# Performance work log

Measured on AMD Instinct MI355X. Metric: run time of the kernel, lower is better.

The kernel has to match this reference:

```python
import jax, jax.numpy as jnp
import numpy as np

T, F, C, V, H, E, S = 256, 32, 8, 10000, 1024, 256, 512
PAD, BOS, EOS = 0, 1, 2


def setup_inputs() -> dict:
    key = jax.random.key(0)
    ks = jax.random.split(key, 16)
    sH = 1.0 / np.sqrt(H).astype(np.float32)
    inp = {
        'token_ctx': jax.random.normal(ks[0], (1, S, H), jnp.float32),
        'char_emb_w': jax.random.normal(ks[1], (V, E), jnp.float32) * 0.02,
        'enc_W_ih': jax.random.normal(ks[2], (3 * H, E), jnp.float32) * sH,
        'enc_W_hh': jax.random.normal(ks[3], (3 * H, H), jnp.float32) * sH,
        'enc_b_ih': jnp.zeros((3 * H,), jnp.float32),
        'enc_b_hh': jnp.zeros((3 * H,), jnp.float32),
        'dec_W_ih': jax.random.normal(ks[4], (3 * H, E), jnp.float32) * sH,
        'dec_W_hh': jax.random.normal(ks[5], (3 * H, H), jnp.float32) * sH,
        'dec_b_ih': jnp.zeros((3 * H,), jnp.float32),
        'dec_b_hh': jnp.zeros((3 * H,), jnp.float32),
        'out_W': jax.random.normal(ks[6], (V, H), jnp.float32) * sH,
        'out_b': jnp.zeros((V,), jnp.float32),
    }
    # (token_id, xtoken_idx, char_id) triples; every token 1..T has exactly C chars
    tok_ids = jnp.repeat(jnp.arange(1, T + 1, dtype=jnp.int32), C)
    xt_ids = jax.random.randint(ks[7], (T * C,), 0, S, jnp.int32)
    ch_ids = jax.random.randint(ks[8], (T * C,), 4, V, jnp.int32)  # avoid specials
    inp['in_sent_token_chars'] = jnp.stack([tok_ids, xt_ids, ch_ids], axis=-1)[None]
    gold = jax.random.randint(ks[9], (T * F,), 4, V, jnp.int32)  # no EOS -> full-length decode
    inp['out_chars'] = jnp.concatenate([jnp.array([BOS], jnp.int32), gold])[None]
    inp['max_tokens'] = T
    inp['max_form_len'] = F
    inp['use_teacher_forcing'] = 1
    return inp


def _gru_cell(x, h, W_ih, W_hh, b_ih, b_hh):
    # PyTorch GRU cell convention; x:[T,E], h:[T,H]
    gi = x @ W_ih.T + b_ih
    gh = h @ W_hh.T + b_hh
    i_r, i_z, i_n = jnp.split(gi, 3, axis=-1)
    h_r, h_z, h_n = jnp.split(gh, 3, axis=-1)
    r = jax.nn.sigmoid(i_r + h_r)
    z = jax.nn.sigmoid(i_z + h_z)
    n = jnp.tanh(i_n + r * h_n)
    return (1.0 - z) * n + z * h


def reference(token_ctx, char_emb_w, enc_W_ih, enc_W_hh, enc_b_ih, enc_b_hh,
              dec_W_ih, dec_W_hh, dec_b_ih, dec_b_hh, out_W, out_b,
              in_sent_token_chars, out_chars, max_tokens, max_form_len,
              use_teacher_forcing):
    Vout = out_b.shape[0]
    # ragged mask select per token id -> here every token has exactly C chars
    tc = in_sent_token_chars[0].reshape(max_tokens, -1, 3)  # [T, C, 3]
    chars = tc[:, :, 2]          # [T, C]
    xtoken_ids = tc[:, :, 1]     # [T, C]
    # enc_state = mean over the token's xtoken contexts
    h0 = jnp.mean(token_ctx[0][xtoken_ids], axis=1)  # [T, H]
    # ---- encoder GRU over the token's chars (batched over tokens) ----
    x_enc = char_emb_w[chars]  # [T, C, E]

    def enc_step(h, x):
        return _gru_cell(x, h, enc_W_ih, enc_W_hh, enc_b_ih, enc_b_hh), None

    h_enc, _ = jax.lax.scan(enc_step, h0, jnp.swapaxes(x_enc, 0, 1))  # [T, H]
    # ---- decoder GRU, max_form_len steps, teacher-forced, EOS freeze+pad ----
    # gold char for token t at step s is out_chars[0, t*F + s + 1]
    gold = out_chars[0, 1:1 + max_tokens * max_form_len].reshape(max_tokens, max_form_len)
    c0 = jnp.full((max_tokens,), out_chars[0, 0], dtype=out_chars.dtype)
    done0 = (c0 == EOS)
    last0 = jnp.zeros((max_tokens, Vout), jnp.float32)

    def dec_step(carry, g):
        h, c, done, last = carry
        x = char_emb_w[c]
        h_new = _gru_cell(x, h, dec_W_ih, dec_W_hh, dec_b_ih, dec_b_hh)
        s_new = h_new @ out_W.T + out_b
        score = jnp.where(done[:, None], last, s_new)  # pad with last score after EOS
        h = jnp.where(done[:, None], h, h_new)         # state frozen after EOS
        if use_teacher_forcing:
            c_next = g
        else:
            c_next = jnp.argmax(s_new, axis=-1).astype(c.dtype)
        done = done | (c_next == EOS)
        return (h, c_next, done, score), score

    _, scores = jax.lax.scan(dec_step, (h_enc, c0, done0, last0),
                             jnp.swapaxes(gold, 0, 1))  # [F, T, V]
    # torch.cat(dec_scores, dim=1): token-major, step-minor -> [1, T*F, V]
    return jnp.transpose(scores, (1, 0, 2)).reshape(1, max_tokens * max_form_len, Vout)
```

## Files before the change

kernel.cpp:

```cpp
#include <hip/hip_runtime.h>
#include <hip/hip_bf16.h>
#include <math.h>

#define TT   256
#define FF   32
#define CCH  8
#define VV   10000
#define HH   1024
#define EE   256
#define NG   3072
#define EOS_ID 2
#define NSTEPS 40
#define CHAIN_BLKS 256
#define CTR_INTS 512

#define LDS_GP_OFF    98304
#define LDS_STB_OFF   (98304 + 53248)
#define LDS_TOTAL     (98304 + 53248 + 2048)

#define SC_LDS_TOTAL  131072

typedef __attribute__((ext_vector_type(8))) short bf16x8;
typedef __attribute__((ext_vector_type(4))) float f32x4;

__device__ __forceinline__ void gload_lds16(const void* g, void* l) {
    __builtin_amdgcn_global_load_lds((const __attribute__((address_space(1))) void*)g,
                                     (__attribute__((address_space(3))) void*)l,
                                     16, 0, 0);
}

__device__ __forceinline__ float sigmf(float x) { return 1.f / (1.f + __expf(-x)); }

__global__ __launch_bounds__(256) void prep_kernel(const int* __restrict__ oc,
                                                   int* __restrict__ c_in,
                                                   unsigned char* __restrict__ done,
                                                   int* __restrict__ ctr) {
    int t = threadIdx.x;
    for (int i = t; i < CTR_INTS; i += 256) ctr[i] = 0;
    int c0 = oc[0];
    bool d = (c0 == EOS_ID);
    for (int f = 0; f < FF; ++f) {
        c_in[t * FF + f] = (f == 0) ? c0 : oc[1 + t * FF + f - 1];
        done[t * FF + f] = d ? 1 : 0;
        d = d || (oc[1 + t * FF + f] == EOS_ID);
    }
}

__global__ __launch_bounds__(256) void h0_kernel(const float* __restrict__ tctx,
                                                 const int* __restrict__ sent,
                                                 float* __restrict__ h,
                                                 __hip_bfloat16* __restrict__ A0) {
    int t = blockIdx.x;
    int tid = threadIdx.x;
    __shared__ int xt[CCH];
    if (tid < CCH) xt[tid] = sent[(t * CCH + tid) * 3 + 1];
    __syncthreads();
#pragma unroll
    for (int jj = 0; jj < 4; ++jj) {
        int j = tid + jj * 256;
        float s = 0.f;
#pragma unroll
        for (int c = 0; c < CCH; ++c) s += tctx[(size_t)xt[c] * HH + j];
        float hv = s * 0.125f;
        h[(size_t)t * HH + j] = hv;
        A0[(size_t)t * HH + j] = __float2bfloat16(hv);
    }
}

__global__ __launch_bounds__(256) void f2b_kernel(const float* __restrict__ src,
                                                  __hip_bfloat16* __restrict__ dst) {
    size_t base = ((size_t)blockIdx.x * 256 + threadIdx.x) * 4;
    float4 v = *(const float4*)(src + base);
    dst[base + 0] = __float2bfloat16(v.x);
    dst[base + 1] = __float2bfloat16(v.y);
    dst[base + 2] = __float2bfloat16(v.z);
    dst[base + 3] = __float2bfloat16(v.w);
}

__global__ __launch_bounds__(256) void build_Bg2(const float* __restrict__ Whh,
                                                 __hip_bfloat16* __restrict__ Bg) {
    int by = blockIdx.x;
    int tid = threadIdx.x;
    int jb = by / 48, rr = by % 48;
    int g = rr >> 4, jj = rr & 15;
    const float* srow = Whh + (size_t)(g * 1024 + jb * 16 + jj) * HH;
    __hip_bfloat16* drow = Bg + (size_t)by * HH;
    float4 v = *(const float4*)(srow + tid * 4);
    drow[tid * 4 + 0] = __float2bfloat16(v.x);
    drow[tid * 4 + 1] = __float2bfloat16(v.y);
    drow[tid * 4 + 2] = __float2bfloat16(v.z);
    drow[tid * 4 + 3] = __float2bfloat16(v.w);
}

template<int MODE>
__global__ __launch_bounds__(256) void gemm_pipe(const __hip_bfloat16* __restrict__ A, int lda,
                                                 const __hip_bfloat16* __restrict__ B, int ldb,
                                                 __hip_bfloat16* __restrict__ Cb,
                                                 const int* __restrict__ idsrc,
                                                 int NIT) {
    __shared__ __hip_bfloat16 As[4][128 * 32];
    __shared__ __hip_bfloat16 Bs[4][128 * 32];
    __shared__ int sids[128];

    const int tid = threadIdx.x;
    const int n0 = blockIdx.x * 128;
    const int m0 = blockIdx.y * 128;

    if (tid < 128) {
        int row = m0 + tid;
        int t = row & 255;
        int id;
        if (MODE == 1) { int c = row >> 8; id = idsrc[(t * CCH + c) * 3 + 2]; }
        else           { int f = row >> 8; id = idsrc[t * FF + f]; }
        sids[tid] = id;
    }
    __syncthreads();

    const int srow = tid >> 2, skq = tid & 3;
    const int l = tid & 63;
    const int w = tid >> 6;
    const int wr = (w >> 1) * 64, wc = (w & 1) * 64;
    const int fra = ((wr + (l & 15)) << 5) + ((l >> 4) << 3);
    const int frb = ((wc + (l & 15)) << 5) + ((l >> 4) << 3);

    f32x4 acc[4][4];
#pragma unroll
    for (int i = 0; i < 4; ++i)
#pragma unroll
        for (int j = 0; j < 4; ++j) acc[i][j] = (f32x4){0.f, 0.f, 0.f, 0.f};

    auto stage = [&](int slot, int it) {
        const int k0 = it * 32;
        const __hip_bfloat16* ga0 = A + (size_t)sids[srow] * lda + k0 + skq * 8;
        const __hip_bfloat16* ga1 = A + (size_t)sids[64 + srow] * lda + k0 + skq * 8;
        const __hip_bfloat16* gb0 = B + (size_t)(n0 + srow) * ldb + k0 + skq * 8;
        const __hip_bfloat16* gb1 = B + (size_t)(n0 + 64 + srow) * ldb + k0 + skq * 8;
        __hip_bfloat16* lA = &As[slot][tid * 8];
        __hip_bfloat16* lB = &Bs[slot][tid * 8];
        gload_lds16(ga0, lA);
        gload_lds16(ga1, lA + 2048);
        gload_lds16(gb0, lB);
        gload_lds16(gb1, lB + 2048);
    };

    stage(0, 0);
    stage(1, 1);

    for (int it = 0; it < NIT; ++it) {
        if (it + 2 < NIT) stage((it + 2) & 3, it + 2);
        int ahead = NIT - 1 - it; if (ahead > 2) ahead = 2;
        if (ahead >= 2)      asm volatile("s_waitcnt vmcnt(8)" ::: "memory");
        else if (ahead == 1) asm volatile("s_waitcnt vmcnt(4)" ::: "memory");
        else                 asm volatile("s_waitcnt vmcnt(0)" ::: "memory");
        __builtin_amdgcn_s_barrier();
        __builtin_amdgcn_sched_barrier(0);

        const __hip_bfloat16* cA = As[it & 3];
        const __hip_bfloat16* cB = Bs[it & 3];
        bf16x8 af[4], bfv[4];
#pragma unroll
        for (int fm = 0; fm < 4; ++fm) af[fm] = *(const bf16x8*)&cA[fra + fm * 512];
#pragma unroll
        for (int fn = 0; fn < 4; ++fn) bfv[fn] = *(const bf16x8*)&cB[frb + fn * 512];
#pragma unroll
        for (int fm = 0; fm < 4; ++fm)
#pragma unroll
            for (int fn = 0; fn < 4; ++fn)
                acc[fm][fn] = __builtin_amdgcn_mfma_f32_16x16x32_bf16(af[fm], bfv[fn], acc[fm][fn], 0, 0, 0);
    }

    const int colb = wc + (l & 15);
    const int rb   = wr + ((l >> 4) << 2);
#pragma unroll
    for (int fm = 0; fm < 4; ++fm)
#pragma unroll
        for (int fn = 0; fn < 4; ++fn)
#pragma unroll
            for (int q = 0; q < 4; ++q)
                Cb[(size_t)(m0 + rb + fm * 16 + q) * NG + n0 + colb + fn * 16] =
                    __float2bfloat16(acc[fm][fn][q]);
}

__global__ __launch_bounds__(256, 1) void chain_kernel(
    __hip_bfloat16* Abuf0, __hip_bfloat16* Abuf1,
    const __hip_bfloat16* __restrict__ Bg_e,
    const __hip_bfloat16* __restrict__ Bg_d,
    const __hip_bfloat16* __restrict__ gi_enc, const __hip_bfloat16* __restrict__ gi_dec,
    const float* __restrict__ ebih, const float* __restrict__ ebhh,
    const float* __restrict__ dbih, const float* __restrict__ dbhh,
    const float* __restrict__ hA,
    __hip_bfloat16* __restrict__ hsb,
    const unsigned char* __restrict__ dflags,
    int* flags) {

    extern __shared__ __align__(16) char smem[];
    char* Bs = smem;
    float* gp = (float*)(smem + LDS_GP_OFF);
    __hip_bfloat16* stb = (__hip_bfloat16*)(smem + LDS_STB_OFF);

    const int tid = threadIdx.x;
    const int b = blockIdx.x;
    const int mt = b >> 6, jb = b & 63;
    const int m0 = mt * 64;
    const int jbase = jb * 16;

    const int l = tid & 63, w = tid >> 6;
    const int ji = tid & 15;
    const int rg = tid >> 4;
    const int j = jbase + ji;
    const int lrow = l & 15;
    const int lk8  = (l >> 4) << 3;

    float hreg[4];
#pragma unroll
    for (int p = 0; p < 4; ++p)
        hreg[p] = hA[(size_t)(m0 + p * 16 + rg) * HH + j];

    const float e_br = ebih[j] + ebhh[j];
    const float e_bz = ebih[HH + j] + ebhh[HH + j];
    const float e_bi = ebih[2 * HH + j];
    const float e_bh = ebhh[2 * HH + j];
    const float d_br = dbih[j] + dbhh[j];
    const float d_bz = dbih[HH + j] + dbhh[HH + j];
    const float d_bi = dbih[2 * HH + j];
    const float d_bh = dbhh[2 * HH + j];

    auto stageBfull = [&](const __hip_bfloat16* Bp) {
#pragma unroll
        for (int c = 0; c < 24; ++c) {
            int chunk = c * 256 + tid;
            int row = chunk >> 7, q = chunk & 127;
            const char* src = (const char*)(Bp + (size_t)row * HH) + ((q ^ (row & 7)) << 4);
            gload_lds16(src, Bs + chunk * 16);
        }
    };

    auto ldB = [&](int nt, int ks) -> bf16x8 {
        int r = nt * 16 + lrow;
        int g = ks * 4 + (l >> 4);
        return *(const bf16x8*)(Bs + r * 2048 + ((g ^ (r & 7)) << 4));
    };

    unsigned int gru[4], gzu[4], gnu[4];
    int dfl[4] = {0, 0, 0, 0};
#pragma unroll
    for (int p = 0; p < 4; ++p) {
        const __hip_bfloat16* gb = gi_enc + (size_t)(m0 + p * 16 + rg) * NG + j;
        asm volatile("global_load_ushort %0, %1, off nt" : "=v"(gru[p]) : "v"(gb));
        asm volatile("global_load_ushort %0, %1, off nt" : "=v"(gzu[p]) : "v"(gb + HH));
        asm volatile("global_load_ushort %0, %1, off nt" : "=v"(gnu[p]) : "v"(gb + 2 * HH));
    }

    for (int s = 0; s < NSTEPS; ++s) {
        if (s > 0) {
            if (tid < 64) {
                const int* fp = flags + (mt << 6) + l;
                long guard = 0;
                for (;;) {
                    int v;
                    asm volatile("global_load_dword %0, %1, off sc0 sc1" : "=v"(v) : "v"(fp));
                    asm volatile("s_waitcnt vmcnt(0)" ::: "memory");
                    if (__all(v >= s)) break;
                    if (++guard > (1L << 22)) break;
                    __builtin_amdgcn_s_sleep(2);
                }
            }
            __syncthreads();
        }

        if (s == 0 || s == CCH) {
            stageBfull(((s == 0) ? Bg_e : Bg_d) + (size_t)jb * 48 * HH);
            asm volatile("s_waitcnt vmcnt(0)" ::: "memory");
            __syncthreads();
        }

        const __hip_bfloat16* Ab = (s & 1) ? Abuf1 : Abuf0;
        __hip_bfloat16* An = (s & 1) ? Abuf0 : Abuf1;

        asm volatile("s_waitcnt vmcnt(0)" ::: "memory");
        const __hip_bfloat16* ap0 = Ab + (size_t)(m0 + 0 * 16 + lrow) * HH + w * 256 + lk8;
        const __hip_bfloat16* ap1 = Ab + (size_t)(m0 + 1 * 16 + lrow) * HH + w * 256 + lk8;
        const __hip_bfloat16* ap2 = Ab + (size_t)(m0 + 2 * 16 + lrow) * HH + w * 256 + lk8;
        const __hip_bfloat16* ap3 = Ab + (size_t)(m0 + 3 * 16 + lrow) * HH + w * 256 + lk8;

        bf16x8 av[8][4];
#pragma unroll
        for (int ksl = 0; ksl < 8; ++ksl) {
            asm volatile("global_load_dwordx4 %0, %1, off sc0 sc1" : "=v"(av[ksl][0]) : "v"(ap0 + ksl * 32));
            asm volatile("global_load_dwordx4 %0, %1, off sc0 sc1" : "=v"(av[ksl][1]) : "v"(ap1 + ksl * 32));
            asm volatile("global_load_dwordx4 %0, %1, off sc0 sc1" : "=v"(av[ksl][2]) : "v"(ap2 + ksl * 32));
            asm volatile("global_load_dwordx4 %0, %1, off sc0 sc1" : "=v"(av[ksl][3]) : "v"(ap3 + ksl * 32));
        }

        f32x4 acc[4][3];
#pragma unroll
        for (int m = 0; m < 4; ++m)
#pragma unroll
            for (int nt = 0; nt < 3; ++nt) acc[m][nt] = (f32x4){0.f, 0.f, 0.f, 0.f};

        const int kbase = w * 8;
        bf16x8 bb[3][3];
#pragma unroll
        for (int nt = 0; nt < 3; ++nt) { bb[0][nt] = ldB(nt, kbase); bb[1][nt] = ldB(nt, kbase + 1); }

#pragma unroll
        for (int ksl = 0; ksl < 8; ++ksl) {
            if (ksl + 2 < 8) {
#pragma unroll
                for (int nt = 0; nt < 3; ++nt) bb[(ksl + 2) % 3][nt] = ldB(nt, kbase + ksl + 2);
            }
            asm volatile("s_waitcnt vmcnt(%0)" :: "i"(28 - 4 * ksl) : "memory");
            __builtin_amdgcn_sched_barrier(0);
#pragma unroll
            for (int m = 0; m < 4; ++m)
#pragma unroll
                for (int nt = 0; nt < 3; ++nt)
                    acc[m][nt] = __builtin_amdgcn_mfma_f32_16x16x32_bf16(av[ksl][m], bb[ksl % 3][nt], acc[m][nt], 0, 0, 0);
        }

        {
            float* gpw = gp + w * (64 * 52);
            const int rbase = (l >> 4) << 2;
#pragma unroll
            for (int m = 0; m < 4; ++m)
#pragma unroll
                for (int nt = 0; nt < 3; ++nt)
#pragma unroll
                    for (int q = 0; q < 4; ++q)
                        gpw[(m * 16 + rbase + q) * 52 + nt * 16 + lrow] = acc[m][nt][q];
        }
        __syncthreads();

        const int f = s - CCH;
        const float br_ = (s < CCH) ? e_br : d_br;
        const float bz_ = (s < CCH) ? e_bz : d_bz;
        const float bi_ = (s < CCH) ? e_bi : d_bi;
        const float bh_ = (s < CCH) ? e_bh : d_bh;
#pragma unroll
        for (int p = 0; p < 4; ++p) {
            const int tr = p * 16 + rg;
            float racc = 0.f, zacc = 0.f, nacc = 0.f;
#pragma unroll
            for (int ww = 0; ww < 4; ++ww) {
                const float* g = gp + ww * (64 * 52) + tr * 52;
                racc += g[ji];
                zacc += g[16 + ji];
                nacc += g[32 + ji];
            }
            float grf = __uint_as_float(gru[p] << 16);
            float gzf = __uint_as_float(gzu[p] << 16);
            float gnf = __uint_as_float(gnu[p] << 16);
            float r = sigmf(grf + br_ + racc);
            float z = sigmf(gzf + bz_ + zacc);
            float n = tanhf(gnf + bi_ + r * (nacc + bh_));
            float hold = hreg[p];
            float hv = (1.f - z) * n + z * hold;
            if (s >= CCH && dfl[p]) hv = hold;
            hreg[p] = hv;
            stb[tr * 16 + ji] = __float2bfloat16(hv);
        }
        __syncthreads();

        if (s < NSTEPS - 1) {
            if (tid < 128) {
                const int row = tid >> 1, part = tid & 1;
                bf16x8 v = *(const bf16x8*)&stb[row * 16 + part * 8];
                const __hip_bfloat16* ap = An + (size_t)(m0 + row) * HH + jbase + part * 8;
                asm volatile("global_store_dwordx4 %0, %1, off sc0 sc1"
                             :: "v"(ap), "v"(v) : "memory");
            }
            asm volatile("s_waitcnt vmcnt(0)" ::: "memory");
            __syncthreads();
            if (tid == 0) {
                int v = s + 1;
                int* fp = flags + (mt << 6) + jb;
                asm volatile("global_store_dword %0, %1, off sc0 sc1"
                             :: "v"(fp), "v"(v) : "memory");
            }
        }
        if (s >= CCH && tid < 128) {
            const int row = tid >> 1, part = tid & 1;
            bf16x8 v = *(const bf16x8*)&stb[row * 16 + part * 8];
            bf16x8* hp = (bf16x8*)(hsb + ((size_t)f * TT + m0 + row) * HH + jbase + part * 8);
            __builtin_nontemporal_store(v, hp);
        }
        if (s < NSTEPS - 1) {
            const __hip_bfloat16* gnext = (s + 1 < CCH) ? (gi_enc + (size_t)(s + 1) * TT * NG)
                                                        : (gi_dec + (size_t)(s + 1 - CCH) * TT * NG);
#pragma unroll
            for (int p = 0; p < 4; ++p) {
                const __hip_bfloat16* gb = gnext + (size_t)(m0 + p * 16 + rg) * NG + j;
                asm volatile("global_load_ushort %0, %1, off nt" : "=v"(gru[p]) : "v"(gb));
                asm volatile("global_load_ushort %0, %1, off nt" : "=v"(gzu[p]) : "v"(gb + HH));
                asm volatile("global_load_ushort %0, %1, off nt" : "=v"(gnu[p]) : "v"(gb + 2 * HH));
            }
            if (s + 1 >= CCH) {
                const int fnx = s + 1 - CCH;
#pragma unroll
                for (int p = 0; p < 4; ++p) {
                    const unsigned char* dp = dflags + (size_t)(m0 + p * 16 + rg) * FF + fnx;
                    asm volatile("global_load_ubyte %0, %1, off" : "=v"(dfl[p]) : "v"(dp));
                }
            }
        }
    }
}

__global__ __launch_bounds__(512, 2) void scores256(const __hip_bfloat16* __restrict__ hsb,
                                                    const __hip_bfloat16* __restrict__ Wb,
                                                    const float* __restrict__ bout,
                                                    const int* __restrict__ oc,
                                                    float* __restrict__ out) {
    extern __shared__ __align__(16) char smem[];

    const int bid = blockIdx.x;
    const int sid = (bid & 7) * 160 + (bid >> 3);
    const int bx = sid % 40, by = sid / 40;
    const int n0 = bx * 256, m0 = by * 256;

    const int tid = threadIdx.x;
    const int l = tid & 63;
    const int w = tid >> 6;
    const int wm = w >> 2;
    const int wn = w & 3;
    const int lrow = l & 15;
    const int qg = l >> 4;

    f32x4 acc[8][4];
#pragma unroll
    for (int i = 0; i < 8; ++i)
#pragma unroll
        for (int j = 0; j < 4; ++j) acc[i][j] = (f32x4){0.f, 0.f, 0.f, 0.f};

    auto stage = [&](int slot, int it) {
        const int k0 = it * 32;
        char* sb = smem + slot * 32768;
#pragma unroll
        for (int cc = 0; cc < 2; ++cc) {
            int chunk = cc * 512 + tid;
            int row = chunk >> 2, q = chunk & 3;
            int qsrc = q ^ (((row >> 1) & 3) ^ (row & 1));
            const __hip_bfloat16* src = hsb + (size_t)(m0 + row) * HH + k0 + qsrc * 8;
            gload_lds16(src, sb + chunk * 16);
        }
#pragma unroll
        for (int cc = 0; cc < 2; ++cc) {
            int chunk = cc * 512 + tid;
            int row = chunk >> 2, q = chunk & 3;
            int br = n0 + row; if (br > VV - 1) br = VV - 1;
            int qsrc = q ^ (((row >> 1) & 3) ^ (row & 1));
            const __hip_bfloat16* src = Wb + (size_t)br * HH + k0 + qsrc * 8;
            gload_lds16(src, sb + 16384 + chunk * 16);
        }
    };

    stage(0, 0);
    stage(1, 1);

    for (int it = 0; it < 32; ++it) {
        if (it + 2 < 32) stage((it + 2) & 3, it + 2);
        int ahead = 31 - it; if (ahead > 2) ahead = 2;
        if (ahead >= 2)      asm volatile("s_waitcnt vmcnt(8)" ::: "memory");
        else if (ahead == 1) asm volatile("s_waitcnt vmcnt(4)" ::: "memory");
        else                 asm volatile("s_waitcnt vmcnt(0)" ::: "memory");
        __builtin_amdgcn_s_barrier();
        __builtin_amdgcn_sched_barrier(0);

        const char* cA = smem + (it & 3) * 32768;
        const char* cB = cA + 16384;
        bf16x8 af[8], bfv[4];
#pragma unroll
        for (int fm = 0; fm < 8; ++fm) {
            int r = wm * 128 + fm * 16 + lrow;
            int qpos = qg ^ (((r >> 1) & 3) ^ (r & 1));
            af[fm] = *(const bf16x8*)(cA + r * 64 + qpos * 16);
        }
#pragma unroll
        for (int fn = 0; fn < 4; ++fn) {
            int r = wn * 64 + fn * 16 + lrow;
            int qpos = qg ^ (((r >> 1) & 3) ^ (r & 1));
            bfv[fn] = *(const bf16x8*)(cB + r * 64 + qpos * 16);
        }
#pragma unroll
        for (int fm = 0; fm < 8; ++fm)
#pragma unroll
            for (int fn = 0; fn < 4; ++fn)
                acc[fm][fn] = __builtin_amdgcn_mfma_f32_16x16x32_bf16(af[fm], bfv[fn], acc[fm][fn], 0, 0, 0);
    }

    const bool zf = (oc[0] == EOS_ID);
    const int colb = wn * 64 + lrow;
    const int rb   = wm * 128 + (qg << 2);
#pragma unroll
    for (int fn = 0; fn < 4; ++fn) {
        int v = n0 + colb + fn * 16;
        if (v < VV) {
            float bb = bout[v];
#pragma unroll
            for (int fm = 0; fm < 8; ++fm) {
#pragma unroll
                for (int q = 0; q < 4; ++q) {
                    int m = m0 + rb + fm * 16 + q;
                    int fo = m >> 8, t = m & 255;
                    float val = zf ? 0.f : (acc[fm][fn][q] + bb);
                    __builtin_nontemporal_store(val, &out[(size_t)(t * FF + fo) * VV + v]);
                }
            }
        }
    }
}

extern "C" void kernel_launch(void* const* d_in, const int* in_sizes, int n_in,
                              void* d_out, int out_size, void* d_ws, size_t ws_size,
                              hipStream_t stream) {
    (void)in_sizes; (void)n_in; (void)ws_size;

    const float* token_ctx = (const float*)d_in[0];
    const float* emb       = (const float*)d_in[1];
    const float* eWih      = (const float*)d_in[2];
    const float* eWhh      = (const float*)d_in[3];
    const float* ebih      = (const float*)d_in[4];
    const float* ebhh      = (const float*)d_in[5];
    const float* dWih      = (const float*)d_in[6];
    const float* dWhh      = (const float*)d_in[7];
    const float* dbih      = (const float*)d_in[8];
    const float* dbhh      = (const float*)d_in[9];
    const float* Wout      = (const float*)d_in[10];
    const float* bout      = (const float*)d_in[11];
    const int*   sent      = (const int*)d_in[12];
    const int*   ochars    = (const int*)d_in[13];
    float* out = (float*)d_out;

    char* w = (char*)d_ws;
    float* hA = (float*)w;                      w += (size_t)TT * HH * 4;
    __hip_bfloat16* Ab0 = (__hip_bfloat16*)w;   w += (size_t)TT * HH * 2;
    __hip_bfloat16* Ab1 = (__hip_bfloat16*)w;   w += (size_t)TT * HH * 2;
    __hip_bfloat16* Woutb = (__hip_bfloat16*)w; w += (size_t)VV * HH * 2;
    int* c_in = (int*)w;                        w += (size_t)TT * FF * 4;
    unsigned char* done = (unsigned char*)w;    w += (size_t)TT * FF;
    w = (char*)(((size_t)w + 255) & ~(size_t)255);
    int* ctr = (int*)w;                         w += (size_t)CTR_INTS * 4;
    __hip_bfloat16* hsb = (__hip_bfloat16*)w;   w += (size_t)FF * TT * HH * 2;

    char* tail = (char*)d_out + (size_t)out_size * 4;
    tail -= (size_t)NG * HH * 2;          __hip_bfloat16* Bg_e = (__hip_bfloat16*)tail;
    tail -= (size_t)NG * HH * 2;          __hip_bfloat16* Bg_d = (__hip_bfloat16*)tail;
    tail -= (size_t)CCH * TT * NG * 2;    __hip_bfloat16* gi_enc = (__hip_bfloat16*)tail;
    tail -= (size_t)FF * TT * NG * 2;     __hip_bfloat16* gi_dec = (__hip_bfloat16*)tail;
    tail -= (size_t)VV * EE * 2;          __hip_bfloat16* emb_bf = (__hip_bfloat16*)tail;
    tail -= (size_t)NG * EE * 2;          __hip_bfloat16* Wihb_e = (__hip_bfloat16*)tail;
    tail -= (size_t)NG * EE * 2;          __hip_bfloat16* Wihb_d = (__hip_bfloat16*)tail;

    hipFuncSetAttribute((const void*)chain_kernel,
                        hipFuncAttributeMaxDynamicSharedMemorySize, LDS_TOTAL);
    hipFuncSetAttribute((const void*)scores256,
                        hipFuncAttributeMaxDynamicSharedMemorySize, SC_LDS_TOTAL);

    prep_kernel<<<1, 256, 0, stream>>>(ochars, c_in, done, ctr);
    h0_kernel<<<TT, 256, 0, stream>>>(token_ctx, sent, hA, Ab0);
    f2b_kernel<<<(VV * EE) / 4 / 256, 256, 0, stream>>>(emb, emb_bf);
    f2b_kernel<<<(NG * EE) / 4 / 256, 256, 0, stream>>>(eWih, Wihb_e);
    f2b_kernel<<<(NG * EE) / 4 / 256, 256, 0, stream>>>(dWih, Wihb_d);
    f2b_kernel<<<(VV * HH) / 4 / 256, 256, 0, stream>>>(Wout, Woutb);
    build_Bg2<<<NG, 256, 0, stream>>>(eWhh, Bg_e);
    build_Bg2<<<NG, 256, 0, stream>>>(dWhh, Bg_d);

    gemm_pipe<1><<<dim3(24, 16), 256, 0, stream>>>(emb_bf, EE, Wihb_e, EE, gi_enc, sent, 8);
    gemm_pipe<2><<<dim3(24, 64), 256, 0, stream>>>(emb_bf, EE, Wihb_d, EE, gi_dec, c_in, 8);

    chain_kernel<<<CHAIN_BLKS, 256, LDS_TOTAL, stream>>>(Ab0, Ab1, Bg_e, Bg_d,
                                                         gi_enc, gi_dec,
                                                         ebih, ebhh, dbih, dbhh,
                                                         hA, hsb, done, ctr);

    scores256<<<1280, 512, SC_LDS_TOTAL, stream>>>(hsb, Woutb, bout, ochars, out);
}
```

Before: 627.8 us.

## Merge prep/convert launches, fuse input GEMMs, re-pipeline scores GEMM with 8-phase schedule

Folds the bf16 conversion kernels, the W_hh reordering and the prep kernel into one launch, and merges the encoder and decoder input-projection GEMMs into one grid. The aim is to cut launch overhead and tail effects. The output-projection GEMM moves to K=64 tiles with a double-buffered, XOR-swizzled LDS layout. Its loop is split into four phases per K-tile that interleave loads with MFMA under s_setprio. The new schedule relies on hand-placed waitcnt and barrier counts and adds more barriers, which raises the risk of synchronisation mistakes.

Result: faster. 601.3 us (-4.2%).

```diff
diff --git a/kernel.cpp b/kernel.cpp
--- a/kernel.cpp
+++ b/kernel.cpp
@@ -31,11 +31,49 @@
 
 __device__ __forceinline__ float sigmf(float x) { return 1.f / (1.f + __expf(-x)); }
 
-__global__ __launch_bounds__(256) void prep_kernel(const int* __restrict__ oc,
-                                                   int* __restrict__ c_in,
-                                                   unsigned char* __restrict__ done,
-                                                   int* __restrict__ ctr) {
-    int t = threadIdx.x;
+__global__ __launch_bounds__(256) void convert_all(
+    const float* __restrict__ emb,  __hip_bfloat16* __restrict__ emb_bf,
+    const float* __restrict__ Wihe, __hip_bfloat16* __restrict__ Wihb_e,
+    const float* __restrict__ Wihd, __hip_bfloat16* __restrict__ Wihb_d,
+    const float* __restrict__ Wout, __hip_bfloat16* __restrict__ Woutb,
+    const float* __restrict__ Whhe, __hip_bfloat16* __restrict__ Bg_e,
+    const float* __restrict__ Whhd, __hip_bfloat16* __restrict__ Bg_d,
+    const int* __restrict__ oc, int* __restrict__ c_in,
+    unsigned char* __restrict__ done, int* __restrict__ ctr) {
+
+    int bx = blockIdx.x;
+    int tid = threadIdx.x;
+
+    const float* src = nullptr; __hip_bfloat16* dst = nullptr; int lb = 0;
+    if (bx < 2500)        { src = emb;  dst = emb_bf;  lb = bx; }
+    else if (bx < 3268)   { src = Wihe; dst = Wihb_e; lb = bx - 2500; }
+    else if (bx < 4036)   { src = Wihd; dst = Wihb_d; lb = bx - 3268; }
+    else if (bx < 14036)  { src = Wout; dst = Woutb;  lb = bx - 4036; }
+    if (src) {
+        size_t base = ((size_t)lb * 256 + tid) * 4;
+        float4 v = *(const float4*)(src + base);
+        dst[base + 0] = __float2bfloat16(v.x);
+        dst[base + 1] = __float2bfloat16(v.y);
+        dst[base + 2] = __float2bfloat16(v.z);
+        dst[base + 3] = __float2bfloat16(v.w);
+        return;
+    }
+    if (bx < 20180) {
+        const float* Whh = (bx < 17108) ? Whhe : Whhd;
+        __hip_bfloat16* Bg = (bx < 17108) ? Bg_e : Bg_d;
+        int by = (bx < 17108) ? (bx - 14036) : (bx - 17108);
+        int jb = by / 48, rr = by % 48;
+        int g = rr >> 4, jj = rr & 15;
+        const float* srow = Whh + (size_t)(g * 1024 + jb * 16 + jj) * HH;
+        __hip_bfloat16* drow = Bg + (size_t)by * HH;
+        float4 v = *(const float4*)(srow + tid * 4);
+        drow[tid * 4 + 0] = __float2bfloat16(v.x);
+        drow[tid * 4 + 1] = __float2bfloat16(v.y);
+        drow[tid * 4 + 2] = __float2bfloat16(v.z);
+        drow[tid * 4 + 3] = __float2bfloat16(v.w);
+        return;
+    }
+    int t = tid;
     for (int i = t; i < CTR_INTS; i += 256) ctr[i] = 0;
     int c0 = oc[0];
     bool d = (c0 == EOS_ID);
@@ -67,51 +105,31 @@
     }
 }
 
-__global__ __launch_bounds__(256) void f2b_kernel(const float* __restrict__ src,
-                                                  __hip_bfloat16* __restrict__ dst) {
-    size_t base = ((size_t)blockIdx.x * 256 + threadIdx.x) * 4;
-    float4 v = *(const float4*)(src + base);
-    dst[base + 0] = __float2bfloat16(v.x);
-    dst[base + 1] = __float2bfloat16(v.y);
-    dst[base + 2] = __float2bfloat16(v.z);
-    dst[base + 3] = __float2bfloat16(v.w);
-}
-
-__global__ __launch_bounds__(256) void build_Bg2(const float* __restrict__ Whh,
-                                                 __hip_bfloat16* __restrict__ Bg) {
-    int by = blockIdx.x;
-    int tid = threadIdx.x;
-    int jb = by / 48, rr = by % 48;
-    int g = rr >> 4, jj = rr & 15;
-    const float* srow = Whh + (size_t)(g * 1024 + jb * 16 + jj) * HH;
-    __hip_bfloat16* drow = Bg + (size_t)by * HH;
-    float4 v = *(const float4*)(srow + tid * 4);
-    drow[tid * 4 + 0] = __float2bfloat16(v.x);
-    drow[tid * 4 + 1] = __float2bfloat16(v.y);
-    drow[tid * 4 + 2] = __float2bfloat16(v.z);
-    drow[tid * 4 + 3] = __float2bfloat16(v.w);
-}
-
-template<int MODE>
-__global__ __launch_bounds__(256) void gemm_pipe(const __hip_bfloat16* __restrict__ A, int lda,
-                                                 const __hip_bfloat16* __restrict__ B, int ldb,
-                                                 __hip_bfloat16* __restrict__ Cb,
-                                                 const int* __restrict__ idsrc,
-                                                 int NIT) {
+__global__ __launch_bounds__(256) void gemm_gi(const __hip_bfloat16* __restrict__ A,
+                                               const __hip_bfloat16* __restrict__ Be,
+                                               const __hip_bfloat16* __restrict__ Bd,
+                                               __hip_bfloat16* __restrict__ Ce,
+                                               __hip_bfloat16* __restrict__ Cd,
+                                               const int* __restrict__ sent,
+                                               const int* __restrict__ c_in) {
     __shared__ __hip_bfloat16 As[4][128 * 32];
     __shared__ __hip_bfloat16 Bs[4][128 * 32];
     __shared__ int sids[128];
 
     const int tid = threadIdx.x;
     const int n0 = blockIdx.x * 128;
-    const int m0 = blockIdx.y * 128;
+    const int byy = blockIdx.y;
+    const bool enc = (byy < 16);
+    const int m0 = (enc ? byy : byy - 16) * 128;
+    const __hip_bfloat16* B = enc ? Be : Bd;
+    __hip_bfloat16* Cb = enc ? Ce : Cd;
 
     if (tid < 128) {
         int row = m0 + tid;
         int t = row & 255;
         int id;
-        if (MODE == 1) { int c = row >> 8; id = idsrc[(t * CCH + c) * 3 + 2]; }
-        else           { int f = row >> 8; id = idsrc[t * FF + f]; }
+        if (enc) { int c = row >> 8; id = sent[(t * CCH + c) * 3 + 2]; }
+        else     { int f = row >> 8; id = c_in[t * FF + f]; }
         sids[tid] = id;
     }
     __syncthreads();
@@ -131,10 +149,10 @@
 
     auto stage = [&](int slot, int it) {
         const int k0 = it * 32;
-        const __hip_bfloat16* ga0 = A + (size_t)sids[srow] * lda + k0 + skq * 8;
-        const __hip_bfloat16* ga1 = A + (size_t)sids[64 + srow] * lda + k0 + skq * 8;
-        const __hip_bfloat16* gb0 = B + (size_t)(n0 + srow) * ldb + k0 + skq * 8;
-        const __hip_bfloat16* gb1 = B + (size_t)(n0 + 64 + srow) * ldb + k0 + skq * 8;
+        const __hip_bfloat16* ga0 = A + (size_t)sids[srow] * EE + k0 + skq * 8;
+        const __hip_bfloat16* ga1 = A + (size_t)sids[64 + srow] * EE + k0 + skq * 8;
+        const __hip_bfloat16* gb0 = B + (size_t)(n0 + srow) * EE + k0 + skq * 8;
+        const __hip_bfloat16* gb1 = B + (size_t)(n0 + 64 + srow) * EE + k0 + skq * 8;
         __hip_bfloat16* lA = &As[slot][tid * 8];
         __hip_bfloat16* lB = &Bs[slot][tid * 8];
         gload_lds16(ga0, lA);
@@ -146,9 +164,9 @@
     stage(0, 0);
     stage(1, 1);
 
-    for (int it = 0; it < NIT; ++it) {
-        if (it + 2 < NIT) stage((it + 2) & 3, it + 2);
-        int ahead = NIT - 1 - it; if (ahead > 2) ahead = 2;
+    for (int it = 0; it < 8; ++it) {
+        if (it + 2 < 8) stage((it + 2) & 3, it + 2);
+        int ahead = 7 - it; if (ahead > 2) ahead = 2;
         if (ahead >= 2)      asm volatile("s_waitcnt vmcnt(8)" ::: "memory");
         else if (ahead == 1) asm volatile("s_waitcnt vmcnt(4)" ::: "memory");
         else                 asm volatile("s_waitcnt vmcnt(0)" ::: "memory");
@@ -406,11 +424,11 @@
     }
 }
 
-__global__ __launch_bounds__(512, 2) void scores256(const __hip_bfloat16* __restrict__ hsb,
-                                                    const __hip_bfloat16* __restrict__ Wb,
-                                                    const float* __restrict__ bout,
-                                                    const int* __restrict__ oc,
-                                                    float* __restrict__ out) {
+__global__ __launch_bounds__(512, 2) void scores8p(const __hip_bfloat16* __restrict__ hsb,
+                                                   const __hip_bfloat16* __restrict__ Wb,
+                                                   const float* __restrict__ bout,
+                                                   const int* __restrict__ oc,
+                                                   float* __restrict__ out) {
     extern __shared__ __align__(16) char smem[];
 
     const int bid = blockIdx.x;
@@ -430,62 +448,132 @@
 #pragma unroll
     for (int i = 0; i < 8; ++i)
 #pragma unroll
-        for (int j = 0; j < 4; ++j) acc[i][j] = (f32x4){0.f, 0.f, 0.f, 0.f};
-
-    auto stage = [&](int slot, int it) {
-        const int k0 = it * 32;
-        char* sb = smem + slot * 32768;
-#pragma unroll
-        for (int cc = 0; cc < 2; ++cc) {
-            int chunk = cc * 512 + tid;
-            int row = chunk >> 2, q = chunk & 3;
-            int qsrc = q ^ (((row >> 1) & 3) ^ (row & 1));
-            const __hip_bfloat16* src = hsb + (size_t)(m0 + row) * HH + k0 + qsrc * 8;
-            gload_lds16(src, sb + chunk * 16);
-        }
-#pragma unroll
-        for (int cc = 0; cc < 2; ++cc) {
-            int chunk = cc * 512 + tid;
-            int row = chunk >> 2, q = chunk & 3;
-            int br = n0 + row; if (br > VV - 1) br = VV - 1;
-            int qsrc = q ^ (((row >> 1) & 3) ^ (row & 1));
-            const __hip_bfloat16* src = Wb + (size_t)br * HH + k0 + qsrc * 8;
-            gload_lds16(src, sb + 16384 + chunk * 16);
+        for (int jj = 0; jj < 4; ++jj) acc[i][jj] = (f32x4){0.f, 0.f, 0.f, 0.f};
+
+    auto stage_half = [&](int h) {
+        const int kt = h >> 2, typ = h & 3;
+        const int k0 = kt * 64;
+        char* base = smem + (kt & 1) * 65536 +
+                     ((typ < 2) ? (32768 + typ * 16384) : ((typ - 2) * 16384));
+#pragma unroll
+        for (int c = 0; c < 2; ++c) {
+            int g = c * 512 + tid;
+            int r = g >> 3, q = g & 7;
+            const __hip_bfloat16* src;
+            if (typ < 2) {
+                int br = n0 + typ * 128 + r; if (br > VV - 1) br = VV - 1;
+                src = Wb + (size_t)br * HH + k0 + ((q ^ (r & 7)) << 3);
+            } else {
+                src = hsb + (size_t)(m0 + (typ - 2) * 128 + r) * HH + k0 + ((q ^ (r & 7)) << 3);
+            }
+            gload_lds16(src, base + g * 16);
         }
     };
 
-    stage(0, 0);
-    stage(1, 1);
-
-    for (int it = 0; it < 32; ++it) {
-        if (it + 2 < 32) stage((it + 2) & 3, it + 2);
-        int ahead = 31 - it; if (ahead > 2) ahead = 2;
-        if (ahead >= 2)      asm volatile("s_waitcnt vmcnt(8)" ::: "memory");
-        else if (ahead == 1) asm volatile("s_waitcnt vmcnt(4)" ::: "memory");
-        else                 asm volatile("s_waitcnt vmcnt(0)" ::: "memory");
-        __builtin_amdgcn_s_barrier();
+    for (int h = 0; h < 6; ++h) stage_half(h);
+    asm volatile("s_waitcnt vmcnt(4)" ::: "memory");
+    __builtin_amdgcn_s_barrier();
+
+    bf16x8 af[4][2], bfv[4][2];
+
+#pragma unroll 1
+    for (int kt = 0; kt < 16; ++kt) {
+        const char* bufb = smem + (kt & 1) * 65536;
+        const char* Abh = bufb + wm * 16384;
+        const char* Bbh = bufb + 32768 + (wn >> 1) * 16384;
+        const int rbB = (wn & 1) * 64;
+
+#pragma unroll
+        for (int fm = 0; fm < 4; ++fm) {
+            int rr = fm * 16 + lrow;
+#pragma unroll
+            for (int ks = 0; ks < 2; ++ks)
+                af[fm][ks] = *(const bf16x8*)(Abh + rr * 128 + (((ks * 4 + qg) ^ (rr & 7)) << 4));
+        }
+#pragma unroll
+        for (int fn = 0; fn < 2; ++fn) {
+            int rr = rbB + fn * 16 + lrow;
+#pragma unroll
+            for (int ks = 0; ks < 2; ++ks)
+                bfv[fn][ks] = *(const bf16x8*)(Bbh + rr * 128 + (((ks * 4 + qg) ^ (rr & 7)) << 4));
+        }
+        if (4 * kt + 6 < 64) stage_half(4 * kt + 6);
+        __builtin_amdgcn_s_barrier();
+        asm volatile("s_waitcnt lgkmcnt(0)" ::: "memory");
         __builtin_amdgcn_sched_barrier(0);
-
-        const char* cA = smem + (it & 3) * 32768;
-        const char* cB = cA + 16384;
-        bf16x8 af[8], bfv[4];
-#pragma unroll
-        for (int fm = 0; fm < 8; ++fm) {
-            int r = wm * 128 + fm * 16 + lrow;
-            int qpos = qg ^ (((r >> 1) & 3) ^ (r & 1));
-            af[fm] = *(const bf16x8*)(cA + r * 64 + qpos * 16);
-        }
-#pragma unroll
-        for (int fn = 0; fn < 4; ++fn) {
-            int r = wn * 64 + fn * 16 + lrow;
-            int qpos = qg ^ (((r >> 1) & 3) ^ (r & 1));
-            bfv[fn] = *(const bf16x8*)(cB + r * 64 + qpos * 16);
-        }
-#pragma unroll
-        for (int fm = 0; fm < 8; ++fm)
-#pragma unroll
-            for (int fn = 0; fn < 4; ++fn)
-                acc[fm][fn] = __builtin_amdgcn_mfma_f32_16x16x32_bf16(af[fm], bfv[fn], acc[fm][fn], 0, 0, 0);
+        __builtin_amdgcn_s_setprio(1);
+#pragma unroll
+        for (int fm = 0; fm < 4; ++fm)
+#pragma unroll
+            for (int fn = 0; fn < 2; ++fn)
+#pragma unroll
+                for (int ks = 0; ks < 2; ++ks)
+                    acc[fm][fn] = __builtin_amdgcn_mfma_f32_16x16x32_bf16(af[fm][ks], bfv[fn][ks], acc[fm][fn], 0, 0, 0);
+        __builtin_amdgcn_s_setprio(0);
+        __builtin_amdgcn_s_barrier();
+
+#pragma unroll
+        for (int fn = 2; fn < 4; ++fn) {
+            int rr = rbB + fn * 16 + lrow;
+#pragma unroll
+            for (int ks = 0; ks < 2; ++ks)
+                bfv[fn][ks] = *(const bf16x8*)(Bbh + rr * 128 + (((ks * 4 + qg) ^ (rr & 7)) << 4));
+        }
+        if (4 * kt + 7 < 64) stage_half(4 * kt + 7);
+        __builtin_amdgcn_s_barrier();
+        asm volatile("s_waitcnt lgkmcnt(0)" ::: "memory");
+        __builtin_amdgcn_sched_barrier(0);
+        __builtin_amdgcn_s_setprio(1);
+#pragma unroll
+        for (int fm = 0; fm < 4; ++fm)
+#pragma unroll
+            for (int fn = 2; fn < 4; ++fn)
+#pragma unroll
+                for (int ks = 0; ks < 2; ++ks)
+                    acc[fm][fn] = __builtin_amdgcn_mfma_f32_16x16x32_bf16(af[fm][ks], bfv[fn][ks], acc[fm][fn], 0, 0, 0);
+        __builtin_amdgcn_s_setprio(0);
+        __builtin_amdgcn_s_barrier();
+
+#pragma unroll
+        for (int fm = 0; fm < 4; ++fm) {
+            int rr = (4 + fm) * 16 + lrow;
+#pragma unroll
+            for (int ks = 0; ks < 2; ++ks)
+                af[fm][ks] = *(const bf16x8*)(Abh + rr * 128 + (((ks * 4 + qg) ^ (rr & 7)) << 4));
+        }
+        if (4 * kt + 8 < 64) stage_half(4 * kt + 8);
+        __builtin_amdgcn_s_barrier();
+        asm volatile("s_waitcnt lgkmcnt(0)" ::: "memory");
+        __builtin_amdgcn_sched_barrier(0);
+        __builtin_amdgcn_s_setprio(1);
+#pragma unroll
+        for (int fm = 0; fm < 4; ++fm)
+#pragma unroll
+            for (int fn = 0; fn < 2; ++fn)
+#pragma unroll
+                for (int ks = 0; ks < 2; ++ks)
+                    acc[4 + fm][fn] = __builtin_amdgcn_mfma_f32_16x16x32_bf16(af[fm][ks], bfv[fn][ks], acc[4 + fm][fn], 0, 0, 0);
+        __builtin_amdgcn_s_setprio(0);
+        __builtin_amdgcn_s_barrier();
+
+        if (4 * kt + 9 < 64) stage_half(4 * kt + 9);
+        if (kt < 15) {
+            if (kt == 14) asm volatile("s_waitcnt vmcnt(0)" ::: "memory");
+            else          asm volatile("s_waitcnt vmcnt(4)" ::: "memory");
+        }
+        __builtin_amdgcn_s_barrier();
+        asm volatile("s_waitcnt lgkmcnt(0)" ::: "memory");
+        __builtin_amdgcn_sched_barrier(0);
+        __builtin_amdgcn_s_setprio(1);
+#pragma unroll
+        for (int fm = 0; fm < 4; ++fm)
+#pragma unroll
+            for (int fn = 2; fn < 4; ++fn)
+#pragma unroll
+                for (int ks = 0; ks < 2; ++ks)
+                    acc[4 + fm][fn] = __builtin_amdgcn_mfma_f32_16x16x32_bf16(af[fm][ks], bfv[fn][ks], acc[4 + fm][fn], 0, 0, 0);
+        __builtin_amdgcn_s_setprio(0);
+        __builtin_amdgcn_s_barrier();
     }
 
     const bool zf = (oc[0] == EOS_ID);
@@ -553,25 +641,21 @@
 
     hipFuncSetAttribute((const void*)chain_kernel,
                         hipFuncAttributeMaxDynamicSharedMemorySize, LDS_TOTAL);
-    hipFuncSetAttribute((const void*)scores256,
+    hipFuncSetAttribute((const void*)scores8p,
                         hipFuncAttributeMaxDynamicSharedMemorySize, SC_LDS_TOTAL);
 
-    prep_kernel<<<1, 256, 0, stream>>>(ochars, c_in, done, ctr);
+    convert_all<<<20181, 256, 0, stream>>>(emb, emb_bf, eWih, Wihb_e, dWih, Wihb_d,
+                                           Wout, Woutb, eWhh, Bg_e, dWhh, Bg_d,
+                                           ochars, c_in, done, ctr);
     h0_kernel<<<TT, 256, 0, stream>>>(token_ctx, sent, hA, Ab0);
-    f2b_kernel<<<(VV * EE) / 4 / 256, 256, 0, stream>>>(emb, emb_bf);
-    f2b_kernel<<<(NG * EE) / 4 / 256, 256, 0, stream>>>(eWih, Wihb_e);
-    f2b_kernel<<<(NG * EE) / 4 / 256, 256, 0, stream>>>(dWih, Wihb_d);
-    f2b_kernel<<<(VV * HH) / 4 / 256, 256, 0, stream>>>(Wout, Woutb);
-    build_Bg2<<<NG, 256, 0, stream>>>(eWhh, Bg_e);
-    build_Bg2<<<NG, 256, 0, stream>>>(dWhh, Bg_d);
-
-    gemm_pipe<1><<<dim3(24, 16), 256, 0, stream>>>(emb_bf, EE, Wihb_e, EE, gi_enc, sent, 8);
-    gemm_pipe<2><<<dim3(24, 64), 256, 0, stream>>>(emb_bf, EE, Wihb_d, EE, gi_dec, c_in, 8);
+
+    gemm_gi<<<dim3(24, 80), 256, 0, stream>>>(emb_bf, Wihb_e, Wihb_d,
+                                              gi_enc, gi_dec, sent, c_in);
 
     chain_kernel<<<CHAIN_BLKS, 256, LDS_TOTAL, stream>>>(Ab0, Ab1, Bg_e, Bg_d,
                                                          gi_enc, gi_dec,
                                                          ebih, ebhh, dbih, dbhh,
                                                          hA, hsb, done, ctr);
 
-    scores256<<<1280, 512, SC_LDS_TOTAL, stream>>>(hsb, Woutb, bout, ochars, out);
+    scores8p<<<1280, 512, SC_LDS_TOTAL, stream>>>(hsb, Woutb, bout, ochars, out);
 }
```
